# Optimization experiments

Measured on AMD Instinct MI355X. Metric: run time of the kernel, lower is better.

Reference implementation:

```python
import jax, jax.numpy as jnp
import numpy as np

D_MODEL = 1024
NUM_HEADS = 16
HEAD_DIM = D_MODEL // NUM_HEADS


def setup_inputs() -> dict:
    key = jax.random.key(0)
    kx, kq, kk, kv, ko = jax.random.split(key, 5)
    B, T = 2, 2048
    scale = 1.0 / np.sqrt(D_MODEL)
    return {
        "x": jax.random.normal(kx, (B, T, D_MODEL), dtype=jnp.float32),
        "wq": jax.random.normal(kq, (D_MODEL, D_MODEL), dtype=jnp.float32) * scale,
        "wk": jax.random.normal(kk, (D_MODEL, D_MODEL), dtype=jnp.float32) * scale,
        "wv": jax.random.normal(kv, (D_MODEL, D_MODEL), dtype=jnp.float32) * scale,
        "wo": jax.random.normal(ko, (D_MODEL, D_MODEL), dtype=jnp.float32) * scale,
    }


def _split_heads(x):
    b, t, _ = x.shape
    return x.reshape(b, t, NUM_HEADS, HEAD_DIM).transpose(0, 2, 1, 3)  # [b,h,t,d]


def reference(x, wq, wk, wv, wo):
    q = _split_heads(x @ wq)
    k = _split_heads(x @ wk)
    v = _split_heads(x @ wv)
    inv_sqrt_d = jnp.asarray(1.0 / np.sqrt(HEAD_DIM), x.dtype)
    scores = jnp.einsum("bhqd,bhkd->bhqk", q, k) * inv_sqrt_d
    weights = jax.nn.softmax(scores, axis=-1)  # dropout rate 0.0 -> identity
    out = jnp.einsum("bhqk,bhkd->bhqd", weights, v)
    b, h, t, d = out.shape
    out = out.transpose(0, 2, 1, 3).reshape(b, t, D_MODEL)
    return out @ wo
```

## Files before the change

### kernel.cpp

```cpp
#include <hip/hip_runtime.h>
#include <stdint.h>

using bf16   = __bf16;
using bf16x8 = __bf16 __attribute__((ext_vector_type(8)));
using bf16x4 = __bf16 __attribute__((ext_vector_type(4)));
using f32x4  = float  __attribute__((ext_vector_type(4)));
using f32x16 = float  __attribute__((ext_vector_type(16)));
using u32x4  = uint32_t __attribute__((ext_vector_type(4)));

#define DM 1024
#define T_ 2048
#define NH 16

__device__ __forceinline__ void gl_lds16(const void* g, void* l) {
  __builtin_amdgcn_global_load_lds(
      (__attribute__((address_space(1))) void*)g,
      (__attribute__((address_space(3))) void*)l, 16, 0, 0);
}

__device__ __forceinline__ f32x4 mfma16(bf16x8 a, bf16x8 b, f32x4 c) {
  return __builtin_amdgcn_mfma_f32_16x16x32_bf16(a, b, c, 0, 0, 0);
}
__device__ __forceinline__ f32x16 mfma32(bf16x8 a, bf16x8 b, f32x16 c) {
  return __builtin_amdgcn_mfma_f32_32x32x16_bf16(a, b, c, 0, 0, 0);
}
__device__ __forceinline__ uint32_t cvtpk(float lo, float hi) {
  uint32_t r;
  asm volatile("v_cvt_pk_bf16_f32 %0, %1, %2" : "=v"(r) : "v"(lo), "v"(hi));
  return r;
}

__global__ __launch_bounds__(256)
void k_prep(const float* __restrict__ x,
            const float* __restrict__ w0, const float* __restrict__ w1,
            const float* __restrict__ w2, const float* __restrict__ w3,
            bf16* __restrict__ xb, bf16* __restrict__ wtq, bf16* __restrict__ wto) {
  __shared__ float tile[64][68];
  const int bid = blockIdx.x;
  if (bid < 2048) {
    const size_t i = (size_t)bid * 256 + threadIdx.x;
    const float4 a = *(const float4*)(x + i * 8);
    const float4 c = *(const float4*)(x + i * 8 + 4);
    bf16x8 v;
    v[0] = (bf16)a.x; v[1] = (bf16)a.y; v[2] = (bf16)a.z; v[3] = (bf16)a.w;
    v[4] = (bf16)c.x; v[5] = (bf16)c.y; v[6] = (bf16)c.z; v[7] = (bf16)c.w;
    *(bf16x8*)(xb + i * 8) = v;
    return;
  }
  const int wblk = bid - 2048;
  const int z = wblk >> 8;
  const int bx = wblk & 15, by = (wblk >> 4) & 15;
  const float* w = (z == 0) ? w0 : (z == 1) ? w1 : (z == 2) ? w2 : w3;
  bf16* wt = (z < 3) ? (wtq + (size_t)z * 1024 * 1024) : wto;
  const float scale = (z == 0) ? 0.125f * 1.44269504f : 1.0f;
  const int tx = threadIdx.x & 15;
  const int ty = threadIdx.x >> 4;
  const int k0 = by * 64, n0 = bx * 64;
#pragma unroll
  for (int j = 0; j < 4; ++j) {
    const int r = ty + 16 * j;
    const float4 v = *(const float4*)(w + (size_t)(k0 + r) * DM + n0 + tx * 4);
    tile[r][tx * 4 + 0] = v.x; tile[r][tx * 4 + 1] = v.y;
    tile[r][tx * 4 + 2] = v.z; tile[r][tx * 4 + 3] = v.w;
  }
  __syncthreads();
#pragma unroll
  for (int j = 0; j < 4; ++j) {
    const int r = ty + 16 * j;
    bf16x4 o;
    o[0] = (bf16)(tile[tx * 4 + 0][r] * scale);
    o[1] = (bf16)(tile[tx * 4 + 1][r] * scale);
    o[2] = (bf16)(tile[tx * 4 + 2][r] * scale);
    o[3] = (bf16)(tile[tx * 4 + 3][r] * scale);
    *(bf16x4*)(wt + (size_t)(n0 + r) * DM + k0 + tx * 4) = o;
  }
}

template<int MODE>
__global__ __launch_bounds__(256)
void k_gemm(const bf16* __restrict__ A, const bf16* __restrict__ BT,
            bf16* __restrict__ Qg, bf16* __restrict__ Kf, bf16* __restrict__ Vf,
            float* __restrict__ Cout) {
  constexpr int BN = (MODE == 0) ? 128 : 64;
  constexpr int NTW = BN / 32;
  constexpr int TNX = (MODE == 0) ? 3 : 2;
  __shared__ __align__(16) bf16 Ash[128 * 32];
  __shared__ __align__(16) bf16 Bsh[BN * 32];
  const int xcd = blockIdx.x & 7, idx = blockIdx.x >> 3;
  const int tn = xcd * TNX + idx % TNX;
  const int tm = idx / TNX;
  const int lane = threadIdx.x & 63, w = threadIdx.x >> 6;
  const int wm = w >> 1, wn = w & 1;
  const int r16 = lane & 15, g = lane >> 4;
  f32x4 acc[4][NTW] = {};
  const bf16* Arow = A + (size_t)tm * 128 * DM;
  const bf16* Brow = BT + (size_t)tn * BN * DM;
  for (int k0 = 0; k0 < DM; k0 += 32) {
#pragma unroll
    for (int t = 0; t < 2; ++t) {
      const int q = t * 256 + w * 64 + lane;
      gl_lds16(Arow + (size_t)(q >> 2) * DM + k0 + (q & 3) * 8, Ash + (t * 256 + w * 64) * 8);
    }
#pragma unroll
    for (int t = 0; t < BN / 64; ++t) {
      const int q = t * 256 + w * 64 + lane;
      gl_lds16(Brow + (size_t)(q >> 2) * DM + k0 + (q & 3) * 8, Bsh + (t * 256 + w * 64) * 8);
    }
    __syncthreads();
    bf16x8 af[4], bfr[NTW];
#pragma unroll
    for (int mt = 0; mt < 4; ++mt)
      af[mt] = *(const bf16x8*)(Ash + (wm * 64 + mt * 16 + r16) * 32 + g * 8);
#pragma unroll
    for (int nt = 0; nt < NTW; ++nt)
      bfr[nt] = *(const bf16x8*)(Bsh + (wn * (BN / 2) + nt * 16 + r16) * 32 + g * 8);
#pragma unroll
    for (int mt = 0; mt < 4; ++mt)
#pragma unroll
      for (int nt = 0; nt < NTW; ++nt)
        acc[mt][nt] = mfma16(af[mt], bfr[nt], acc[mt][nt]);
    __syncthreads();
  }
#pragma unroll
  for (int mt = 0; mt < 4; ++mt) {
#pragma unroll
    for (int nt = 0; nt < NTW; ++nt) {
      const int ncol = tn * BN + wn * (BN / 2) + nt * 16 + r16;
      const int m0 = tm * 128 + wm * 64 + mt * 16 + g * 4;
      if (MODE == 0) {
        const int which = ncol >> 10, nl = ncol & 1023;
        const int h = nl >> 6, d = nl & 63;
        const int b = m0 >> 11, t0 = m0 & 2047;
        const size_t hb = (size_t)(b * NH + h) * (T_ * 64);
        if (which == 2) {
          const int kt = t0 >> 6, s = (t0 & 63) >> 4, hi2 = (t0 >> 3) & 1, j0 = t0 & 7;
          const int dh = d >> 5, d31 = d & 31;
          bf16x4 pv;
#pragma unroll
          for (int r = 0; r < 4; ++r) pv[r] = (bf16)acc[mt][nt][r];
          *(bf16x4*)(Vf + hb + kt * 4096 + (s * 2 + dh) * 512 + (hi2 * 32 + d31) * 8 + j0) = pv;
        } else if (which == 1) {
          const int kt = t0 >> 6, kh2 = (t0 >> 5) & 1;
          const int s = d >> 4, hi2 = (d >> 3) & 1, j = d & 7;
          bf16* base = Kf + hb + kt * 4096 + (s * 2 + kh2) * 512 + hi2 * 256 + j;
#pragma unroll
          for (int r = 0; r < 4; ++r)
            base[((t0 & 31) + r) * 8] = (bf16)acc[mt][nt][r];
        } else {
#pragma unroll
          for (int r = 0; r < 4; ++r)
            Qg[hb + (size_t)(t0 + r) * 64 + d] = (bf16)acc[mt][nt][r];
        }
      } else {
#pragma unroll
        for (int r = 0; r < 4; ++r)
          Cout[(size_t)(m0 + r) * DM + ncol] = acc[mt][nt][r];
      }
    }
  }
}

__global__ __launch_bounds__(512)
void k_attn(const bf16* __restrict__ Qg, const bf16* __restrict__ Kf,
            const bf16* __restrict__ Vf, bf16* __restrict__ Ao) {
  __shared__ __align__(16) bf16 Ksh[2][2][64 * 64];
  __shared__ __align__(16) bf16 Vsh[2][2][64 * 64];
  __shared__ float Lsh[4][64];
  const int lin = ((blockIdx.x & 7) << 6) | (blockIdx.x >> 3);
  const int bh = lin >> 4, qt = lin & 15;
  const int lane = threadIdx.x & 63, w = threadIdx.x >> 6;
  const int qw = w & 3, kh = w >> 2;
  const int l31 = lane & 31, hi = lane >> 5;
  const bf16* Qb  = Qg + (size_t)bh * T_ * 64;
  const bf16* Kfh = Kf + (size_t)bh * T_ * 64;
  const bf16* Vfh = Vf + (size_t)bh * T_ * 64;
  const int q0 = qt * 128 + qw * 32;
  bf16x8 qb[4];
#pragma unroll
  for (int s = 0; s < 4; ++s)
    qb[s] = *(const bf16x8*)(Qb + (size_t)(q0 + l31) * 64 + s * 16 + hi * 8);
  f32x16 o0 = {}, o1 = {};
  float llocal = 0.f;

  auto stage = [&](int buf, int ti) {
#pragma unroll
    for (int j = 0; j < 2; ++j) {
      const int idx = qw * 2 + j;
      gl_lds16(Kfh + (size_t)ti * 4096 + idx * 512 + lane * 8, &Ksh[kh][buf][idx * 512]);
      gl_lds16(Vfh + (size_t)ti * 4096 + idx * 512 + lane * 8, &Vsh[kh][buf][idx * 512]);
    }
  };
  auto pvstep = [&](const f32x16& sv, int si, const bf16* Vc, int s) {
    uint32_t a0 = cvtpk(sv[si + 0], sv[si + 1]);
    uint32_t a1 = cvtpk(sv[si + 2], sv[si + 3]);
    uint32_t b0 = cvtpk(sv[si + 4], sv[si + 5]);
    uint32_t b1 = cvtpk(sv[si + 6], sv[si + 7]);
    asm volatile("v_permlane32_swap_b32 %0, %1" : "+v"(a0), "+v"(b0));
    asm volatile("v_permlane32_swap_b32 %0, %1" : "+v"(a1), "+v"(b1));
    u32x4 fr; fr[0] = a0; fr[1] = a1; fr[2] = b0; fr[3] = b1;
    const bf16x8 pas = __builtin_bit_cast(bf16x8, fr);
    const bf16x8 v0 = *(const bf16x8*)(Vc + (s * 2 + 0) * 512 + lane * 8);
    const bf16x8 v1 = *(const bf16x8*)(Vc + (s * 2 + 1) * 512 + lane * 8);
    o0 = mfma32(pas, v0, o0);
    o1 = mfma32(pas, v1, o1);
  };

  constexpr int NTH = T_ / 64 / 2;
  stage(0, kh * NTH);
  __syncthreads();
  for (int i = 0; i < NTH; ++i) {
    const int cur = i & 1;
    if (i + 1 < NTH) stage(cur ^ 1, kh * NTH + i + 1);
    const bf16* Kc = &Ksh[kh][cur][0];
    const bf16* Vc = &Vsh[kh][cur][0];
    f32x16 st0 = {}, st1 = {};
    __builtin_amdgcn_s_setprio(1);
#pragma unroll
    for (int s = 0; s < 4; ++s) {
      const bf16x8 k0 = *(const bf16x8*)(Kc + (s * 2 + 0) * 512 + lane * 8);
      st0 = mfma32(k0, qb[s], st0);
    }
#pragma unroll
    for (int s = 0; s < 4; ++s) {
      const bf16x8 k1 = *(const bf16x8*)(Kc + (s * 2 + 1) * 512 + lane * 8);
      st1 = mfma32(k1, qb[s], st1);
    }
    __builtin_amdgcn_s_setprio(0);
#pragma unroll
    for (int r = 0; r < 16; ++r) {
      st0[r] = __builtin_amdgcn_exp2f(st0[r]); llocal += st0[r];
    }
    __builtin_amdgcn_s_setprio(1);
    pvstep(st0, 0, Vc, 0);
    pvstep(st0, 8, Vc, 1);
    __builtin_amdgcn_s_setprio(0);
#pragma unroll
    for (int r = 0; r < 16; ++r) {
      st1[r] = __builtin_amdgcn_exp2f(st1[r]); llocal += st1[r];
    }
    __builtin_amdgcn_s_setprio(1);
    pvstep(st1, 0, Vc, 2);
    pvstep(st1, 8, Vc, 3);
    __builtin_amdgcn_s_setprio(0);
    __syncthreads();
  }
  float* cb = (float*)&Ksh[0][0][0] + qw * 2048;
  if (kh == 1) {
#pragma unroll
    for (int r = 0; r < 16; ++r) {
      cb[r * 64 + lane]        = o0[r];
      cb[(16 + r) * 64 + lane] = o1[r];
    }
    Lsh[qw][lane] = llocal;
  }
  __syncthreads();
  if (kh == 0) {
    llocal += Lsh[qw][lane];
#pragma unroll
    for (int r = 0; r < 16; ++r) {
      o0[r] += cb[r * 64 + lane];
      o1[r] += cb[(16 + r) * 64 + lane];
    }
    llocal += __shfl_xor(llocal, 32);
    const int b = bh >> 4, h = bh & 15;
#pragma unroll
    for (int r = 0; r < 16; ++r) {
      const int qoff = (r & 3) + 8 * (r >> 2) + 4 * hi;
      const float linv = 1.f / __shfl(llocal, qoff);
      const size_t base = ((size_t)(b * T_ + q0 + qoff)) * DM + h * 64 + l31;
      Ao[base]      = (bf16)(o0[r] * linv);
      Ao[base + 32] = (bf16)(o1[r] * linv);
    }
  }
}

extern "C" void kernel_launch(void* const* d_in, const int* in_sizes, int n_in,
                              void* d_out, int out_size, void* d_ws, size_t ws_size,
                              hipStream_t stream) {
  const float* x  = (const float*)d_in[0];
  const float* wq = (const float*)d_in[1];
  const float* wk = (const float*)d_in[2];
  const float* wv = (const float*)d_in[3];
  const float* wo = (const float*)d_in[4];
  char* ws = (char*)d_ws;
  const size_t MB = 1024 * 1024;
  bf16* xb   = (bf16*)(ws + 0);
  bf16* wtq  = (bf16*)(ws + 8 * MB);
  bf16* wto  = (bf16*)(ws + 14 * MB);
  bf16* Qg   = (bf16*)(ws + 16 * MB);
  bf16* Kfb  = (bf16*)(ws + 24 * MB);
  bf16* Vfb  = (bf16*)(ws + 32 * MB);

  k_prep<<<dim3(3072), dim3(256), 0, stream>>>(x, wq, wk, wv, wo, xb, wtq, wto);
  k_gemm<0><<<dim3(768), dim3(256), 0, stream>>>(xb, wtq, Qg, Kfb, Vfb, (float*)nullptr);
  k_attn<<<dim3(512), dim3(512), 0, stream>>>(Qg, Kfb, Vfb, xb);
  k_gemm<1><<<dim3(512), dim3(256), 0, stream>>>(xb, wto, (bf16*)nullptr, (bf16*)nullptr,
                                                 (bf16*)nullptr, (float*)d_out);
}
```

Before: 119.0 us.

## Use 256x256 double-buffered 8-wave QKV GEMM; split sum accumulators in attention

Replaces the QKV projection GEMM with a new kernel that uses 256x256 tiles, 512 threads and double-buffered LDS staging over 64-wide k steps. Global loads are interleaved with MFMA groups under explicit waitcnt and barriers. Larger tiles give more data reuse per LDS load and fewer blocks (192 instead of 768), but leave fewer blocks than CUs, which hurts occupancy and wave balance. The attention kernel also splits its softmax row-sum into four independent accumulators to shorten the add dependency chain. The output GEMM is specialised into its own kernel with unchanged behaviour.

```diff
diff --git a/kernel.cpp b/kernel.cpp
--- a/kernel.cpp
+++ b/kernel.cpp
@@ -76,14 +76,135 @@
   }
 }
 
-template<int MODE>
+#define DOMFMA(MG)                                                        \
+  do {                                                                    \
+    __builtin_amdgcn_s_setprio(1);                                        \
+    _Pragma("unroll") for (int ms = 0; ms < 4; ++ms)                      \
+      _Pragma("unroll") for (int ns = 0; ns < 4; ++ns)                    \
+        acc[(MG) * 4 + ms][ns] =                                          \
+            mfma16(af[ms], bfr[ns], acc[(MG) * 4 + ms][ns]);              \
+    __builtin_amdgcn_s_setprio(0);                                        \
+  } while (0)
+
+__global__ __launch_bounds__(512, 2)
+void k_gemm8(const bf16* __restrict__ A, const bf16* __restrict__ BT,
+             bf16* __restrict__ Qg, bf16* __restrict__ Kf, bf16* __restrict__ Vf) {
+  __shared__ __align__(16) bf16 Ash[2][2][256 * 32];
+  __shared__ __align__(16) bf16 Bsh[2][2][256 * 32];
+  const int tm = blockIdx.x / 12, tn = blockIdx.x % 12;
+  const int tid = threadIdx.x;
+  const int lane = tid & 63, w = tid >> 6;
+  const int wr = w >> 2, wc = w & 3;
+  const int r16 = lane & 15, g = lane >> 4;
+  f32x4 acc[8][4] = {};
+  const bf16* Ab = A + (size_t)tm * 256 * DM;
+  const bf16* Bb = BT + (size_t)tn * 256 * DM;
+
+  auto stageA = [&](int buf, int kt, int kh) {
+#pragma unroll
+    for (int j = 0; j < 2; ++j) {
+      const int c = tid + 512 * j;
+      gl_lds16(Ab + (size_t)(c >> 2) * DM + kt * 64 + kh * 32 + (c & 3) * 8,
+               &Ash[buf][kh][(w * 64 + 512 * j) * 8]);
+    }
+  };
+  auto stageB = [&](int buf, int kt, int kh) {
+#pragma unroll
+    for (int j = 0; j < 2; ++j) {
+      const int c = tid + 512 * j;
+      gl_lds16(Bb + (size_t)(c >> 2) * DM + kt * 64 + kh * 32 + (c & 3) * 8,
+               &Bsh[buf][kh][(w * 64 + 512 * j) * 8]);
+    }
+  };
+  bf16x8 af[4], bfr[4];
+  auto ldA = [&](int buf, int kh, int mgrp) {
+#pragma unroll
+    for (int ms = 0; ms < 4; ++ms) {
+      const int row = wr * 128 + mgrp * 64 + ms * 16 + r16;
+      af[ms] = *(const bf16x8*)(&Ash[buf][kh][row * 32 + g * 8]);
+    }
+  };
+  auto ldB = [&](int buf, int kh) {
+#pragma unroll
+    for (int ns = 0; ns < 4; ++ns) {
+      const int row = wc * 64 + ns * 16 + r16;
+      bfr[ns] = *(const bf16x8*)(&Bsh[buf][kh][row * 32 + g * 8]);
+    }
+  };
+
+  stageA(0, 0, 0); stageB(0, 0, 0); stageA(0, 0, 1); stageB(0, 0, 1);
+  asm volatile("s_waitcnt vmcnt(4)" ::: "memory");
+  __builtin_amdgcn_s_barrier();
+#pragma unroll 1
+  for (int kt = 0; kt < 15; ++kt) {
+    const int cur = kt & 1, nxt = cur ^ 1;
+    ldB(cur, 0); ldA(cur, 0, 0);
+    stageA(nxt, kt + 1, 0);
+    DOMFMA(0);
+    asm volatile("" ::: "memory");
+    __builtin_amdgcn_s_barrier();
+    ldA(cur, 0, 1);
+    stageB(nxt, kt + 1, 0);
+    DOMFMA(1);
+    asm volatile("s_waitcnt vmcnt(4)" ::: "memory");
+    __builtin_amdgcn_s_barrier();
+    ldB(cur, 1); ldA(cur, 1, 0);
+    stageA(nxt, kt + 1, 1);
+    DOMFMA(0);
+    asm volatile("" ::: "memory");
+    __builtin_amdgcn_s_barrier();
+    ldA(cur, 1, 1);
+    stageB(nxt, kt + 1, 1);
+    DOMFMA(1);
+    asm volatile("s_waitcnt vmcnt(4)" ::: "memory");
+    __builtin_amdgcn_s_barrier();
+  }
+  asm volatile("s_waitcnt vmcnt(0)" ::: "memory");
+  __builtin_amdgcn_s_barrier();
+  ldB(1, 0); ldA(1, 0, 0); DOMFMA(0);
+  ldA(1, 0, 1);            DOMFMA(1);
+  ldB(1, 1); ldA(1, 1, 0); DOMFMA(0);
+  ldA(1, 1, 1);            DOMFMA(1);
+
+#pragma unroll
+  for (int ms = 0; ms < 8; ++ms) {
+#pragma unroll
+    for (int ns = 0; ns < 4; ++ns) {
+      const int ncol = tn * 256 + wc * 64 + ns * 16 + r16;
+      const int m0 = tm * 256 + wr * 128 + ms * 16 + g * 4;
+      const int which = ncol >> 10, nl = ncol & 1023;
+      const int h = nl >> 6, d = nl & 63;
+      const int b = m0 >> 11, t0 = m0 & 2047;
+      const size_t hb = (size_t)(b * NH + h) * (T_ * 64);
+      if (which == 2) {
+        const int kt = t0 >> 6, s = (t0 & 63) >> 4, hi2 = (t0 >> 3) & 1, j0 = t0 & 7;
+        const int dh = d >> 5, d31 = d & 31;
+        bf16x4 pv;
+#pragma unroll
+        for (int r = 0; r < 4; ++r) pv[r] = (bf16)acc[ms][ns][r];
+        *(bf16x4*)(Vf + hb + kt * 4096 + (s * 2 + dh) * 512 + (hi2 * 32 + d31) * 8 + j0) = pv;
+      } else if (which == 1) {
+        const int kt = t0 >> 6, kh2 = (t0 >> 5) & 1;
+        const int s = d >> 4, hi2 = (d >> 3) & 1, j = d & 7;
+        bf16* base = Kf + hb + kt * 4096 + (s * 2 + kh2) * 512 + hi2 * 256 + j;
+#pragma unroll
+        for (int r = 0; r < 4; ++r)
+          base[((t0 & 31) + r) * 8] = (bf16)acc[ms][ns][r];
+      } else {
+#pragma unroll
+        for (int r = 0; r < 4; ++r)
+          Qg[hb + (size_t)(t0 + r) * 64 + d] = (bf16)acc[ms][ns][r];
+      }
+    }
+  }
+}
+
 __global__ __launch_bounds__(256)
-void k_gemm(const bf16* __restrict__ A, const bf16* __restrict__ BT,
-            bf16* __restrict__ Qg, bf16* __restrict__ Kf, bf16* __restrict__ Vf,
-            float* __restrict__ Cout) {
-  constexpr int BN = (MODE == 0) ? 128 : 64;
-  constexpr int NTW = BN / 32;
-  constexpr int TNX = (MODE == 0) ? 3 : 2;
+void k_gemm1(const bf16* __restrict__ A, const bf16* __restrict__ BT,
+             float* __restrict__ Cout) {
+  constexpr int BN = 64;
+  constexpr int NTW = 2;
+  constexpr int TNX = 2;
   __shared__ __align__(16) bf16 Ash[128 * 32];
   __shared__ __align__(16) bf16 Bsh[BN * 32];
   const int xcd = blockIdx.x & 7, idx = blockIdx.x >> 3;
@@ -101,10 +222,9 @@
       const int q = t * 256 + w * 64 + lane;
       gl_lds16(Arow + (size_t)(q >> 2) * DM + k0 + (q & 3) * 8, Ash + (t * 256 + w * 64) * 8);
     }
-#pragma unroll
-    for (int t = 0; t < BN / 64; ++t) {
-      const int q = t * 256 + w * 64 + lane;
-      gl_lds16(Brow + (size_t)(q >> 2) * DM + k0 + (q & 3) * 8, Bsh + (t * 256 + w * 64) * 8);
+    {
+      const int q = w * 64 + lane;
+      gl_lds16(Brow + (size_t)(q >> 2) * DM + k0 + (q & 3) * 8, Bsh + (w * 64) * 8);
     }
     __syncthreads();
     bf16x8 af[4], bfr[NTW];
@@ -127,35 +247,9 @@
     for (int nt = 0; nt < NTW; ++nt) {
       const int ncol = tn * BN + wn * (BN / 2) + nt * 16 + r16;
       const int m0 = tm * 128 + wm * 64 + mt * 16 + g * 4;
-      if (MODE == 0) {
-        const int which = ncol >> 10, nl = ncol & 1023;
-        const int h = nl >> 6, d = nl & 63;
-        const int b = m0 >> 11, t0 = m0 & 2047;
-        const size_t hb = (size_t)(b * NH + h) * (T_ * 64);
-        if (which == 2) {
-          const int kt = t0 >> 6, s = (t0 & 63) >> 4, hi2 = (t0 >> 3) & 1, j0 = t0 & 7;
-          const int dh = d >> 5, d31 = d & 31;
-          bf16x4 pv;
-#pragma unroll
-          for (int r = 0; r < 4; ++r) pv[r] = (bf16)acc[mt][nt][r];
-          *(bf16x4*)(Vf + hb + kt * 4096 + (s * 2 + dh) * 512 + (hi2 * 32 + d31) * 8 + j0) = pv;
-        } else if (which == 1) {
-          const int kt = t0 >> 6, kh2 = (t0 >> 5) & 1;
-          const int s = d >> 4, hi2 = (d >> 3) & 1, j = d & 7;
-          bf16* base = Kf + hb + kt * 4096 + (s * 2 + kh2) * 512 + hi2 * 256 + j;
-#pragma unroll
-          for (int r = 0; r < 4; ++r)
-            base[((t0 & 31) + r) * 8] = (bf16)acc[mt][nt][r];
-        } else {
-#pragma unroll
-          for (int r = 0; r < 4; ++r)
-            Qg[hb + (size_t)(t0 + r) * 64 + d] = (bf16)acc[mt][nt][r];
-        }
-      } else {
-#pragma unroll
-        for (int r = 0; r < 4; ++r)
-          Cout[(size_t)(m0 + r) * DM + ncol] = acc[mt][nt][r];
-      }
+#pragma unroll
+      for (int r = 0; r < 4; ++r)
+        Cout[(size_t)(m0 + r) * DM + ncol] = acc[mt][nt][r];
     }
   }
 }
@@ -180,7 +274,7 @@
   for (int s = 0; s < 4; ++s)
     qb[s] = *(const bf16x8*)(Qb + (size_t)(q0 + l31) * 64 + s * 16 + hi * 8);
   f32x16 o0 = {}, o1 = {};
-  float llocal = 0.f;
+  float lacc0 = 0.f, lacc1 = 0.f, lacc2 = 0.f, lacc3 = 0.f;
 
   auto stage = [&](int buf, int ti) {
 #pragma unroll
@@ -227,16 +321,22 @@
     }
     __builtin_amdgcn_s_setprio(0);
 #pragma unroll
-    for (int r = 0; r < 16; ++r) {
-      st0[r] = __builtin_amdgcn_exp2f(st0[r]); llocal += st0[r];
+    for (int r = 0; r < 16; r += 4) {
+      st0[r + 0] = __builtin_amdgcn_exp2f(st0[r + 0]); lacc0 += st0[r + 0];
+      st0[r + 1] = __builtin_amdgcn_exp2f(st0[r + 1]); lacc1 += st0[r + 1];
+      st0[r + 2] = __builtin_amdgcn_exp2f(st0[r + 2]); lacc2 += st0[r + 2];
+      st0[r + 3] = __builtin_amdgcn_exp2f(st0[r + 3]); lacc3 += st0[r + 3];
     }
     __builtin_amdgcn_s_setprio(1);
     pvstep(st0, 0, Vc, 0);
     pvstep(st0, 8, Vc, 1);
     __builtin_amdgcn_s_setprio(0);
 #pragma unroll
-    for (int r = 0; r < 16; ++r) {
-      st1[r] = __builtin_amdgcn_exp2f(st1[r]); llocal += st1[r];
+    for (int r = 0; r < 16; r += 4) {
+      st1[r + 0] = __builtin_amdgcn_exp2f(st1[r + 0]); lacc0 += st1[r + 0];
+      st1[r + 1] = __builtin_amdgcn_exp2f(st1[r + 1]); lacc1 += st1[r + 1];
+      st1[r + 2] = __builtin_amdgcn_exp2f(st1[r + 2]); lacc2 += st1[r + 2];
+      st1[r + 3] = __builtin_amdgcn_exp2f(st1[r + 3]); lacc3 += st1[r + 3];
     }
     __builtin_amdgcn_s_setprio(1);
     pvstep(st1, 0, Vc, 2);
@@ -244,6 +344,7 @@
     __builtin_amdgcn_s_setprio(0);
     __syncthreads();
   }
+  float llocal = (lacc0 + lacc1) + (lacc2 + lacc3);
   float* cb = (float*)&Ksh[0][0][0] + qw * 2048;
   if (kh == 1) {
 #pragma unroll
@@ -292,8 +393,7 @@
   bf16* Vfb  = (bf16*)(ws + 32 * MB);
 
   k_prep<<<dim3(3072), dim3(256), 0, stream>>>(x, wq, wk, wv, wo, xb, wtq, wto);
-  k_gemm<0><<<dim3(768), dim3(256), 0, stream>>>(xb, wtq, Qg, Kfb, Vfb, (float*)nullptr);
+  k_gemm8<<<dim3(192), dim3(512), 0, stream>>>(xb, wtq, Qg, Kfb, Vfb);
   k_attn<<<dim3(512), dim3(512), 0, stream>>>(Qg, Kfb, Vfb, xb);
-  k_gemm<1><<<dim3(512), dim3(256), 0, stream>>>(xb, wto, (bf16*)nullptr, (bf16*)nullptr,
-                                                 (bf16*)nullptr, (float*)d_out);
-}
+  k_gemm1<<<dim3(512), dim3(256), 0, stream>>>(xb, wto, (float*)d_out);
+}
```

Measured after the change: 120.5 us. Within noise of the previous version (+1.2%).
